# Performance work log

Measured on AMD Instinct MI355X. Metric: run time of the kernel, lower is better.

## Reference

```python
import jax, jax.numpy as jnp
import numpy as np

LN_EPS = 1e-5

def _ln(x, g, b):
    mu = x.mean(-1, keepdims=True)
    var = ((x - mu) ** 2).mean(-1, keepdims=True)
    return (x - mu) * jax.lax.rsqrt(var + LN_EPS) * g + b

def _gru(x, h, wih, whh, bih, bhh):
    # torch GRUCell: gates ordered (r, z, n)
    gi = x @ wih.T + bih
    gh = h @ whh.T + bhh
    ir, iz, inn = jnp.split(gi, 3, axis=-1)
    hr, hz, hn = jnp.split(gh, 3, axis=-1)
    r = jax.nn.sigmoid(ir + hr)
    z = jax.nn.sigmoid(iz + hz)
    n = jnp.tanh(inn + r * hn)
    return (1.0 - z) * n + z * h

def setup_inputs() -> dict:
    key = jax.random.key(0)
    ks = jax.random.split(key, 10)
    B, N, D, S, H = 64, 4096, 128, 8, 256
    w = D ** -0.5  # weight scale to keep activations sane
    return {
        'inputs': jax.random.normal(ks[0], (B, N, D), jnp.float32),
        'slot_noise': jax.random.normal(ks[1], (1, S, D), jnp.float32),
        'slots_mu': jax.random.normal(ks[2], (1, S, D), jnp.float32) * w,
        'slots_log_sigma': jnp.zeros((1, S, D), jnp.float32),
        'wq': jax.random.normal(ks[3], (D, D), jnp.float32) * w,
        'bq': jnp.zeros((D,), jnp.float32),
        'wk': jax.random.normal(ks[4], (D, D), jnp.float32) * w,
        'bk': jnp.zeros((D,), jnp.float32),
        'wv': jax.random.normal(ks[5], (D, D), jnp.float32) * w,
        'bv': jnp.zeros((D,), jnp.float32),
        'gru_wih': jax.random.normal(ks[6], (3 * D, D), jnp.float32) * w,
        'gru_whh': jax.random.normal(ks[7], (3 * D, D), jnp.float32) * w,
        'gru_bih': jnp.zeros((3 * D,), jnp.float32),
        'gru_bhh': jnp.zeros((3 * D,), jnp.float32),
        'ns_g': jnp.ones((D,), jnp.float32),
        'ns_b': jnp.zeros((D,), jnp.float32),
        'ni_g': jnp.ones((D,), jnp.float32),
        'ni_b': jnp.zeros((D,), jnp.float32),
        'mlp_ln_g': jnp.ones((D,), jnp.float32),
        'mlp_ln_b': jnp.zeros((D,), jnp.float32),
        'mlp_w1': jax.random.normal(ks[8], (H, D), jnp.float32) * w,
        'mlp_b1': jnp.zeros((H,), jnp.float32),
        'mlp_w2': jax.random.normal(ks[9], (D, H), jnp.float32) * (H ** -0.5),
        'mlp_b2': jnp.zeros((D,), jnp.float32),
    }

N_ITERS = 3

def reference(inputs, slot_noise, slots_mu, slots_log_sigma, wq, bq, wk, bk, wv, bv,
              gru_wih, gru_whh, gru_bih, gru_bhh, ns_g, ns_b, ni_g, ni_b,
              mlp_ln_g, mlp_ln_b, mlp_w1, mlp_b1, mlp_w2, mlp_b2):
    B, N, D = inputs.shape
    S = slots_mu.shape[1]
    slots = slots_mu + jnp.exp(slots_log_sigma) * slot_noise  # [1,S,D]
    slots = jnp.broadcast_to(slots, (B, S, D))
    x = _ln(inputs, ni_g, ni_b)
    k = x @ wk.T + bk  # [B,N,D]
    v = x @ wv.T + bv
    scale = 1.0 / jnp.sqrt(jnp.float32(D))
    for _ in range(N_ITERS):
        q = _ln(slots, ns_g, ns_b) @ wq.T + bq  # [B,S,D]
        logits = jnp.einsum('bnd,bsd->bns', k, q) * scale
        attn = jax.nn.softmax(logits, axis=-1)  # softmax over slots
        attn_norm = jnp.clip(attn.sum(axis=1, keepdims=True), 1e-8, None)
        slot_attn = attn / attn_norm
        updates = jnp.einsum('bns,bnd->bsd', slot_attn, v)
        slots = _gru(updates, slots, gru_wih, gru_whh, gru_bih, gru_bhh)
        h = jax.nn.gelu(_ln(slots, mlp_ln_g, mlp_ln_b) @ mlp_w1.T + mlp_b1, approximate=False)
        slots = slots + (h @ mlp_w2.T + mlp_b2)
    return slots
```

## Files before the change

kernel.cpp:

```cpp
#include <hip/hip_runtime.h>
#include <hip/hip_bf16.h>
#include <math.h>

#define Bn 64
#define Nn 4096
#define Dn 128
#define Sn 8
#define Hn 256
#define LN_EPS 1e-5f
#define KS_S 136
#define QSCALE 0.08838834764831845f

typedef __bf16 bf16x8 __attribute__((ext_vector_type(8)));
typedef float f32x4 __attribute__((ext_vector_type(4)));
typedef unsigned short ushort_t;

__device__ __forceinline__ float dot4(float4 a, float4 b) {
    return a.x*b.x + a.y*b.y + a.z*b.z + a.w*b.w;
}
__device__ __forceinline__ ushort_t f2bf(float f) {
    __bf16 b = (__bf16)f;
    ushort_t u; __builtin_memcpy(&u, &b, 2); return u;
}
__device__ __forceinline__ float bf2f(ushort_t u) {
    unsigned int x = ((unsigned int)u) << 16; float f; __builtin_memcpy(&f, &x, 4); return f;
}
__device__ __forceinline__ bf16x8 zero8() {
    bf16x8 z;
    #pragma unroll
    for (int i = 0; i < 8; ++i) z[i] = (__bf16)0.0f;
    return z;
}

__global__ void k_slots_init(const float* __restrict__ mu, const float* __restrict__ ls,
                             const float* __restrict__ noise, float* __restrict__ slots) {
    int i = blockIdx.x * blockDim.x + threadIdx.x;
    if (i < Sn * Dn) {
        float v = mu[i] + __expf(ls[i]) * noise[i];
        #pragma unroll 4
        for (int b = 0; b < Bn; ++b) slots[b * Sn * Dn + i] = v;
    }
}

__global__ void k_wprep(const float* __restrict__ wk, const float* __restrict__ wv,
                        ushort_t* __restrict__ wallT) {
    int o = blockIdx.x * blockDim.x + threadIdx.x;
    if (o < 32768) {
        int e = o & 7;
        int l = (o >> 3) & 15;
        int q = (o >> 7) & 3;
        int k = (o >> 9) & 3;
        int G = o >> 11;
        int row = G * 16 + l;
        int col = k * 32 + q * 8 + e;
        float f = (row < 128) ? wk[row * 128 + col] : wv[(row - 128) * 128 + col];
        wallT[o] = f2bf(f);
    }
}

__global__ __launch_bounds__(256) void k_lnkv_mfma(
    const float* __restrict__ inp, const float* __restrict__ ni_g, const float* __restrict__ ni_b,
    const ushort_t* __restrict__ wallT, const float* __restrict__ bk, const float* __restrict__ bv,
    ushort_t* __restrict__ kout, ushort_t* __restrict__ vout)
{
    __shared__ ushort_t xs[64 * KS_S];
    __shared__ float stats[128];
    __shared__ float gb[256];
    const int t = threadIdx.x;
    const int rowbase = blockIdx.x * 64;

    gb[t] = (t < 128) ? ni_g[t] : ni_b[t - 128];

    const float* src = inp + (size_t)rowbase * Dn;
    float4 xv[8];
    #pragma unroll
    for (int it = 0; it < 8; ++it) {
        int f = it * 256 + t;
        float4 x4 = ((const float4*)src)[f];
        xv[it] = x4;
        float s  = x4.x + x4.y + x4.z + x4.w;
        float sq = x4.x*x4.x + x4.y*x4.y + x4.z*x4.z + x4.w*x4.w;
        #pragma unroll
        for (int m = 1; m <= 16; m <<= 1) { s += __shfl_xor(s, m); sq += __shfl_xor(sq, m); }
        if ((t & 31) == 0) {
            int r = it * 8 + (t >> 5);
            float mu  = s * (1.0f / 128.0f);
            float var = sq * (1.0f / 128.0f) - mu * mu;
            stats[2 * r]     = mu;
            stats[2 * r + 1] = rsqrtf(var + LN_EPS);
        }
    }
    __syncthreads();
    #pragma unroll
    for (int it = 0; it < 8; ++it) {
        int f = it * 256 + t;
        int r = f >> 5;
        int c = (f & 31) * 4;
        float mu = stats[2 * r], rs = stats[2 * r + 1];
        float4 x4 = xv[it];
        ushort4 o = { f2bf((x4.x - mu) * rs * gb[c + 0] + gb[128 + c + 0]),
                      f2bf((x4.y - mu) * rs * gb[c + 1] + gb[128 + c + 1]),
                      f2bf((x4.z - mu) * rs * gb[c + 2] + gb[128 + c + 2]),
                      f2bf((x4.w - mu) * rs * gb[c + 3] + gb[128 + c + 3]) };
        *(ushort4*)&xs[r * KS_S + c] = o;
    }
    __syncthreads();

    const int lane = t & 63;
    const int w = t >> 6;
    const int colw = w * 64;
    const int l15 = lane & 15, q = lane >> 4;
    const bool is_k = (colw < 128);
    const int b_idx = rowbase >> 12;
    const int nloc0 = rowbase & 4095;

    bf16x8 afr[4][4];
    #pragma unroll
    for (int ct = 0; ct < 4; ++ct) {
        int G = w * 4 + ct;
        #pragma unroll
        for (int k = 0; k < 4; ++k)
            afr[ct][k] = *(const bf16x8*)&wallT[(size_t)((G * 4 + k) * 64 + lane) * 8];
    }
    float4 biask[4];
    float biasv[4];
    #pragma unroll
    for (int ct = 0; ct < 4; ++ct) {
        if (is_k) biask[ct] = *(const float4*)&bk[colw + ct * 16 + q * 4];
        else      biasv[ct] = bv[colw - 128 + ct * 16 + l15];
    }

    #pragma unroll
    for (int rt = 0; rt < 4; ++rt) {
        bf16x8 bfr[4];
        #pragma unroll
        for (int k = 0; k < 4; ++k)
            bfr[k] = *(const bf16x8*)&xs[(rt * 16 + l15) * KS_S + k * 32 + q * 8];
        #pragma unroll
        for (int ct = 0; ct < 4; ++ct) {
            f32x4 acc = {0.f, 0.f, 0.f, 0.f};
            if (is_k) {
                #pragma unroll
                for (int k = 0; k < 4; ++k)
                    acc = __builtin_amdgcn_mfma_f32_16x16x32_bf16(afr[ct][k], bfr[k], acc, 0, 0, 0);
                int d0 = colw + ct * 16 + q * 4;
                int c  = d0 >> 5;
                int qd = (d0 >> 3) & 3;
                int e0 = d0 & 7;
                ushort4 o = { f2bf(acc[0] + biask[ct].x), f2bf(acc[1] + biask[ct].y),
                              f2bf(acc[2] + biask[ct].z), f2bf(acc[3] + biask[ct].w) };
                size_t off = ((size_t)(((rowbase >> 4) + rt) * 4 + c) * 64 + qd * 16 + l15) * 8 + e0;
                *(ushort4*)&kout[off] = o;
            } else {
                #pragma unroll
                for (int k = 0; k < 4; ++k)
                    acc = __builtin_amdgcn_mfma_f32_16x16x32_bf16(bfr[k], afr[ct][k], acc, 0, 0, 0);
                int dgrp = (w - 2) * 4 + ct;
                int n0 = nloc0 + rt * 16 + q * 4;
                int nc = n0 >> 5;
                int qn = (n0 >> 3) & 3;
                int e0 = n0 & 7;
                float bb = biasv[ct];
                ushort4 o = { f2bf(acc[0] + bb), f2bf(acc[1] + bb),
                              f2bf(acc[2] + bb), f2bf(acc[3] + bb) };
                size_t off = (((size_t)(b_idx * 8 + dgrp) * 128 + nc) * 64 + qn * 16 + l15) * 8 + e0;
                *(ushort4*)&vout[off] = o;
            }
        }
    }
}

__global__ __launch_bounds__(256) void k_qproj2(
    const float* __restrict__ slots, const float* __restrict__ ns_g, const float* __restrict__ ns_b,
    const float* __restrict__ wq, const float* __restrict__ bq,
    ushort_t* __restrict__ qb)
{
    __shared__ float lnq[8][128];
    const int t = threadIdx.x;
    const int bs0 = blockIdx.x * 8;
    {
        int r = t >> 5, c = (t & 31) * 4;
        float4 x4 = *(const float4*)&slots[(size_t)(bs0 + r) * Dn + c];
        float s  = x4.x + x4.y + x4.z + x4.w;
        float sq = x4.x*x4.x + x4.y*x4.y + x4.z*x4.z + x4.w*x4.w;
        #pragma unroll
        for (int m = 1; m <= 16; m <<= 1) { s += __shfl_xor(s, m); sq += __shfl_xor(sq, m); }
        float mu = s * (1.0f / 128.0f);
        float rs = rsqrtf(sq * (1.0f / 128.0f) - mu * mu + LN_EPS);
        lnq[r][c+0] = (x4.x - mu) * rs * ns_g[c+0] + ns_b[c+0];
        lnq[r][c+1] = (x4.y - mu) * rs * ns_g[c+1] + ns_b[c+1];
        lnq[r][c+2] = (x4.z - mu) * rs * ns_g[c+2] + ns_b[c+2];
        lnq[r][c+3] = (x4.w - mu) * rs * ns_g[c+3] + ns_b[c+3];
    }
    __syncthreads();
    {
        int c = t & 127, rb = (t >> 7) * 4;
        const float* W = wq + (size_t)c * Dn;
        float acc[4] = {0.f, 0.f, 0.f, 0.f};
        for (int d = 0; d < 128; d += 4) {
            float4 w4 = *(const float4*)(W + d);
            #pragma unroll
            for (int rr = 0; rr < 4; ++rr) acc[rr] += dot4(w4, *(const float4*)&lnq[rb + rr][d]);
        }
        float bb = bq[c];
        #pragma unroll
        for (int rr = 0; rr < 4; ++rr)
            qb[(size_t)(bs0 + rb + rr) * Dn + c] = f2bf((acc[rr] + bb) * QSCALE);
    }
}

__global__ __launch_bounds__(256) void k_attn_mfma(
    const ushort_t* __restrict__ kbuf, const ushort_t* __restrict__ vtbuf,
    const ushort_t* __restrict__ qb,
    float* __restrict__ upart, float* __restrict__ npart)
{
    __shared__ ushort_t ps[16 * KS_S];
    __shared__ float nsh[8];
    const int t = threadIdx.x;
    const int b = blockIdx.y;
    const int chunk = blockIdx.x;
    const int lane = t & 63;
    const int w = t >> 6;
    const int l15 = lane & 15;
    const int q = lane >> 4;

    for (int i = t; i < 8 * KS_S; i += 256) ps[8 * KS_S + i] = 0;
    if (t < 8) nsh[t] = 0.f;

    bf16x8 aq[4];
    #pragma unroll
    for (int c = 0; c < 4; ++c) {
        bf16x8 z = zero8();
        if (l15 < 8)
            z = *(const bf16x8*)&qb[((size_t)b * Sn + l15) * Dn + c * 32 + q * 8];
        aq[c] = z;
    }

    f32x4 acc[2];
    acc[0] = (f32x4){0.f, 0.f, 0.f, 0.f};
    acc[1] = (f32x4){0.f, 0.f, 0.f, 0.f};
    float nacc[4] = {0.f, 0.f, 0.f, 0.f};

    for (int nt = 0; nt < 4; ++nt) {
        __syncthreads();
        #pragma unroll
        for (int g = 0; g < 2; ++g) {
            int ng = chunk * 32 + nt * 8 + w * 2 + g;
            f32x4 lg = {0.f, 0.f, 0.f, 0.f};
            #pragma unroll
            for (int c = 0; c < 4; ++c) {
                bf16x8 bk = *(const bf16x8*)&kbuf[(((size_t)b * 256 + ng) * 4 + c) * 512 + lane * 8];
                lg = __builtin_amdgcn_mfma_f32_16x16x32_bf16(aq[c], bk, lg, 0, 0, 0);
            }
            int nloc = w * 32 + g * 16 + l15;
            float mown = fmaxf(fmaxf(lg[0], lg[1]), fmaxf(lg[2], lg[3]));
            float m8 = fmaxf(mown, __shfl_xor(mown, 16));
            float p0 = __expf(lg[0] - m8), p1 = __expf(lg[1] - m8);
            float p2 = __expf(lg[2] - m8), p3 = __expf(lg[3] - m8);
            float sown = p0 + p1 + p2 + p3;
            float inv = 1.0f / (sown + __shfl_xor(sown, 16));
            if (q < 2) {
                ushort_t u0 = f2bf(p0 * inv), u1 = f2bf(p1 * inv);
                ushort_t u2 = f2bf(p2 * inv), u3 = f2bf(p3 * inv);
                int s0 = q * 4;
                ps[(s0 + 0) * KS_S + nloc] = u0;
                ps[(s0 + 1) * KS_S + nloc] = u1;
                ps[(s0 + 2) * KS_S + nloc] = u2;
                ps[(s0 + 3) * KS_S + nloc] = u3;
                nacc[0] += bf2f(u0); nacc[1] += bf2f(u1);
                nacc[2] += bf2f(u2); nacc[3] += bf2f(u3);
            }
        }
        __syncthreads();

        bf16x8 pa[4];
        #pragma unroll
        for (int c = 0; c < 4; ++c)
            pa[c] = *(const bf16x8*)&ps[l15 * KS_S + c * 32 + q * 8];

        #pragma unroll
        for (int g2 = 0; g2 < 2; ++g2) {
            int dgrp = w * 2 + g2;
            #pragma unroll
            for (int c = 0; c < 4; ++c) {
                int nc = chunk * 16 + nt * 4 + c;
                bf16x8 bv = *(const bf16x8*)&vtbuf[(((size_t)b * 8 + dgrp) * 128 + nc) * 512 + lane * 8];
                acc[g2] = __builtin_amdgcn_mfma_f32_16x16x32_bf16(pa[c], bv, acc[g2], 0, 0, 0);
            }
        }
    }

    if (q < 2) {
        #pragma unroll
        for (int r = 0; r < 4; ++r) {
            float v = nacc[r];
            v += __shfl_xor(v, 1); v += __shfl_xor(v, 2);
            v += __shfl_xor(v, 4); v += __shfl_xor(v, 8);
            if (l15 == 0) atomicAdd(&nsh[q * 4 + r], v);
        }
        #pragma unroll
        for (int g2 = 0; g2 < 2; ++g2) {
            int d = w * 32 + g2 * 16 + l15;
            #pragma unroll
            for (int r = 0; r < 4; ++r)
                upart[((size_t)(chunk * 64 + b) * 8 + q * 4 + r) * 128 + d] = acc[g2][r];
        }
    }
    __syncthreads();
    if (t < 8) npart[chunk * 512 + b * 8 + t] = nsh[t];
}

__global__ __launch_bounds__(256) void k_update3(
    const float* __restrict__ slots,
    const float* __restrict__ upart, const float* __restrict__ npart,
    const float* __restrict__ wih, const float* __restrict__ whh,
    const float* __restrict__ bih, const float* __restrict__ bhh,
    const float* __restrict__ mlg, const float* __restrict__ mlb,
    const float* __restrict__ w1, const float* __restrict__ b1,
    const float* __restrict__ w2, const float* __restrict__ b2,
    const float* __restrict__ ns_g, const float* __restrict__ ns_b,
    const float* __restrict__ wq, const float* __restrict__ bq,
    float* __restrict__ outp, ushort_t* __restrict__ qb, int do_q)
{
    __shared__ float us[128];
    __shared__ float hs[128];
    __shared__ float gs[768];
    __shared__ float hnw[128];
    __shared__ float lns[128];
    __shared__ float h1s[256];
    const int t = threadIdx.x;
    const int bs = blockIdx.x;

    if (t < 128) {
        float u = 0.f;
        #pragma unroll
        for (int c = 0; c < 8; ++c) u += upart[((size_t)(c * 512 + bs)) * 128 + t];
        float nsum = 0.f;
        #pragma unroll
        for (int c = 0; c < 8; ++c) nsum += npart[c * 512 + bs];
        us[t] = u / fmaxf(nsum, 1e-8f);
        hs[t] = slots[(size_t)bs * Dn + t];
    }
    __syncthreads();

    #pragma unroll
    for (int jj = 0; jj < 3; ++jj) {
        int j = t + jj * 256;
        const float* W = (j < 384) ? (wih + (size_t)j * Dn) : (whh + (size_t)(j - 384) * Dn);
        const float* X = (j < 384) ? us : hs;
        float a = 0.f;
        #pragma unroll 8
        for (int d = 0; d < 128; d += 4)
            a += dot4(*(const float4*)(W + d), *(const float4*)(X + d));
        gs[j] = a;
    }
    __syncthreads();

    if (t < 64) {
        float hnew[2];
        #pragma unroll
        for (int e = 0; e < 2; ++e) {
            int i = t + e * 64;
            float ir = gs[i]       + bih[i],       hr = gs[384 + i] + bhh[i];
            float iz = gs[128 + i] + bih[128 + i], hz = gs[512 + i] + bhh[128 + i];
            float in_= gs[256 + i] + bih[256 + i], hn = gs[640 + i] + bhh[256 + i];
            float r = 1.0f / (1.0f + __expf(-(ir + hr)));
            float z = 1.0f / (1.0f + __expf(-(iz + hz)));
            float n = tanhf(in_ + r * hn);
            hnew[e] = (1.0f - z) * n + z * hs[i];
        }
        float s  = hnew[0] + hnew[1];
        float sq = hnew[0]*hnew[0] + hnew[1]*hnew[1];
        #pragma unroll
        for (int m = 1; m <= 32; m <<= 1) { s += __shfl_xor(s, m); sq += __shfl_xor(sq, m); }
        float mu = s * (1.0f / 128.0f);
        float rs = rsqrtf(sq * (1.0f / 128.0f) - mu * mu + LN_EPS);
        #pragma unroll
        for (int e = 0; e < 2; ++e) {
            int i = t + e * 64;
            hnw[i] = hnew[e];
            lns[i] = (hnew[e] - mu) * rs * mlg[i] + mlb[i];
        }
    }
    __syncthreads();

    {
        const float* W = w1 + (size_t)t * Dn;
        float a = 0.f;
        #pragma unroll 8
        for (int d = 0; d < 128; d += 4)
            a += dot4(*(const float4*)(W + d), *(const float4*)&lns[d]);
        float x = a + b1[t];
        h1s[t] = 0.5f * x * (1.0f + erff(x * 0.70710678118654752f));
    }
    __syncthreads();

    if (t < 128) {
        const float* W = w2 + (size_t)t * Hn;
        float a = 0.f;
        #pragma unroll 8
        for (int d = 0; d < 256; d += 4)
            a += dot4(*(const float4*)(W + d), *(const float4*)&h1s[d]);
        float o = hnw[t] + a + b2[t];
        outp[(size_t)bs * Dn + t] = o;
        us[t] = o;
    }
    if (do_q) {
        __syncthreads();
        if (t < 64) {
            float v0 = us[t], v1 = us[t + 64];
            float s  = v0 + v1;
            float sq = v0*v0 + v1*v1;
            #pragma unroll
            for (int m = 1; m <= 32; m <<= 1) { s += __shfl_xor(s, m); sq += __shfl_xor(sq, m); }
            float mu = s * (1.0f / 128.0f);
            float rs = rsqrtf(sq * (1.0f / 128.0f) - mu * mu + LN_EPS);
            lns[t]      = (v0 - mu) * rs * ns_g[t]      + ns_b[t];
            lns[t + 64] = (v1 - mu) * rs * ns_g[t + 64] + ns_b[t + 64];
        }
        __syncthreads();
        if (t < 128) {
            const float* W = wq + (size_t)t * Dn;
            float a = 0.f;
            #pragma unroll 8
            for (int d = 0; d < 128; d += 4)
                a += dot4(*(const float4*)(W + d), *(const float4*)&lns[d]);
            qb[(size_t)bs * Dn + t] = f2bf((a + bq[t]) * QSCALE);
        }
    }
}

extern "C" void kernel_launch(void* const* d_in, const int* in_sizes, int n_in,
                              void* d_out, int out_size, void* d_ws, size_t ws_size,
                              hipStream_t stream) {
    (void)in_sizes; (void)n_in; (void)out_size; (void)ws_size;
    const float* inputs   = (const float*)d_in[0];
    const float* noise    = (const float*)d_in[1];
    const float* slots_mu = (const float*)d_in[2];
    const float* slots_ls = (const float*)d_in[3];
    const float* wq  = (const float*)d_in[4];
    const float* bq  = (const float*)d_in[5];
    const float* wk  = (const float*)d_in[6];
    const float* bk  = (const float*)d_in[7];
    const float* wv  = (const float*)d_in[8];
    const float* bv  = (const float*)d_in[9];
    const float* gwih = (const float*)d_in[10];
    const float* gwhh = (const float*)d_in[11];
    const float* gbih = (const float*)d_in[12];
    const float* gbhh = (const float*)d_in[13];
    const float* ns_g = (const float*)d_in[14];
    const float* ns_b = (const float*)d_in[15];
    const float* ni_g = (const float*)d_in[16];
    const float* ni_b = (const float*)d_in[17];
    const float* mlg  = (const float*)d_in[18];
    const float* mlb  = (const float*)d_in[19];
    const float* mw1  = (const float*)d_in[20];
    const float* mb1  = (const float*)d_in[21];
    const float* mw2  = (const float*)d_in[22];
    const float* mb2  = (const float*)d_in[23];

    float* ws      = (float*)d_ws;
    float* slots   = ws;
    float* upart   = ws + 65536;
    float* npart   = ws + 590336;
    ushort_t* qb    = (ushort_t*)(ws + 594432);
    ushort_t* wallT = (ushort_t*)(ws + 627200);
    ushort_t* kbuf  = (ushort_t*)(ws + 655360);
    ushort_t* vtbuf = (ushort_t*)(ws + 655360 + 16777216);

    k_slots_init<<<4, 256, 0, stream>>>(slots_mu, slots_ls, noise, slots);
    k_wprep<<<128, 256, 0, stream>>>(wk, wv, wallT);
    k_lnkv_mfma<<<4096, 256, 0, stream>>>(inputs, ni_g, ni_b, wallT, bk, bv, kbuf, vtbuf);
    k_qproj2<<<64, 256, 0, stream>>>(slots, ns_g, ns_b, wq, bq, qb);
    for (int iter = 0; iter < 3; ++iter) {
        k_attn_mfma<<<dim3(8, 64), 256, 0, stream>>>(kbuf, vtbuf, qb, upart, npart);
        float* outp = (iter == 2) ? (float*)d_out : slots;
        k_update3<<<512, 256, 0, stream>>>(slots, upart, npart, gwih, gwhh, gbih, gbhh,
                                           mlg, mlb, mw1, mb1, mw2, mb2, ns_g, ns_b, wq, bq,
                                           outp, qb, (iter == 2) ? 0 : 1);
    }
}
```

Baseline: 481.3 us.

## Keep LN and attention probabilities in registers, drop LDS staging and syncs

The LN+KV projection kernel now has each wave normalise its own 16 rows directly into MFMA B-fragments in registers, instead of staging through LDS. Each wave then loops over all 16 output column tiles, reloading weight fragments from global memory. The attention kernel moves to 512 threads, computes softmax over slots with lane shuffles, and builds the P fragment by shuffles rather than an LDS round trip. Partial updates are reduced across waves in LDS at the end, which removes per-tile barriers and the atomics but adds a larger shared buffer and more weight traffic per block.

```diff
diff --git a/kernel.cpp b/kernel.cpp
--- a/kernel.cpp
+++ b/kernel.cpp
@@ -8,7 +8,6 @@
 #define Sn 8
 #define Hn 256
 #define LN_EPS 1e-5f
-#define KS_S 136
 #define QSCALE 0.08838834764831845f
 
 typedef __bf16 bf16x8 __attribute__((ext_vector_type(8)));
@@ -63,109 +62,82 @@
     const ushort_t* __restrict__ wallT, const float* __restrict__ bk, const float* __restrict__ bv,
     ushort_t* __restrict__ kout, ushort_t* __restrict__ vout)
 {
-    __shared__ ushort_t xs[64 * KS_S];
-    __shared__ float stats[128];
-    __shared__ float gb[256];
     const int t = threadIdx.x;
-    const int rowbase = blockIdx.x * 64;
-
-    gb[t] = (t < 128) ? ni_g[t] : ni_b[t - 128];
-
-    const float* src = inp + (size_t)rowbase * Dn;
-    float4 xv[8];
-    #pragma unroll
-    for (int it = 0; it < 8; ++it) {
-        int f = it * 256 + t;
-        float4 x4 = ((const float4*)src)[f];
-        xv[it] = x4;
-        float s  = x4.x + x4.y + x4.z + x4.w;
-        float sq = x4.x*x4.x + x4.y*x4.y + x4.z*x4.z + x4.w*x4.w;
-        #pragma unroll
-        for (int m = 1; m <= 16; m <<= 1) { s += __shfl_xor(s, m); sq += __shfl_xor(sq, m); }
-        if ((t & 31) == 0) {
-            int r = it * 8 + (t >> 5);
-            float mu  = s * (1.0f / 128.0f);
-            float var = sq * (1.0f / 128.0f) - mu * mu;
-            stats[2 * r]     = mu;
-            stats[2 * r + 1] = rsqrtf(var + LN_EPS);
-        }
-    }
-    __syncthreads();
-    #pragma unroll
-    for (int it = 0; it < 8; ++it) {
-        int f = it * 256 + t;
-        int r = f >> 5;
-        int c = (f & 31) * 4;
-        float mu = stats[2 * r], rs = stats[2 * r + 1];
-        float4 x4 = xv[it];
-        ushort4 o = { f2bf((x4.x - mu) * rs * gb[c + 0] + gb[128 + c + 0]),
-                      f2bf((x4.y - mu) * rs * gb[c + 1] + gb[128 + c + 1]),
-                      f2bf((x4.z - mu) * rs * gb[c + 2] + gb[128 + c + 2]),
-                      f2bf((x4.w - mu) * rs * gb[c + 3] + gb[128 + c + 3]) };
-        *(ushort4*)&xs[r * KS_S + c] = o;
-    }
-    __syncthreads();
-
     const int lane = t & 63;
     const int w = t >> 6;
-    const int colw = w * 64;
     const int l15 = lane & 15, q = lane >> 4;
-    const bool is_k = (colw < 128);
+    const int rowbase = blockIdx.x * 64;
+    const int row = rowbase + w * 16 + l15;
     const int b_idx = rowbase >> 12;
-    const int nloc0 = rowbase & 4095;
-
-    bf16x8 afr[4][4];
-    #pragma unroll
-    for (int ct = 0; ct < 4; ++ct) {
-        int G = w * 4 + ct;
-        #pragma unroll
-        for (int k = 0; k < 4; ++k)
-            afr[ct][k] = *(const bf16x8*)&wallT[(size_t)((G * 4 + k) * 64 + lane) * 8];
-    }
-    float4 biask[4];
-    float biasv[4];
-    #pragma unroll
-    for (int ct = 0; ct < 4; ++ct) {
-        if (is_k) biask[ct] = *(const float4*)&bk[colw + ct * 16 + q * 4];
-        else      biasv[ct] = bv[colw - 128 + ct * 16 + l15];
-    }
-
-    #pragma unroll
-    for (int rt = 0; rt < 4; ++rt) {
-        bf16x8 bfr[4];
-        #pragma unroll
-        for (int k = 0; k < 4; ++k)
-            bfr[k] = *(const bf16x8*)&xs[(rt * 16 + l15) * KS_S + k * 32 + q * 8];
-        #pragma unroll
-        for (int ct = 0; ct < 4; ++ct) {
-            f32x4 acc = {0.f, 0.f, 0.f, 0.f};
-            if (is_k) {
-                #pragma unroll
-                for (int k = 0; k < 4; ++k)
-                    acc = __builtin_amdgcn_mfma_f32_16x16x32_bf16(afr[ct][k], bfr[k], acc, 0, 0, 0);
-                int d0 = colw + ct * 16 + q * 4;
-                int c  = d0 >> 5;
-                int qd = (d0 >> 3) & 3;
-                int e0 = d0 & 7;
-                ushort4 o = { f2bf(acc[0] + biask[ct].x), f2bf(acc[1] + biask[ct].y),
-                              f2bf(acc[2] + biask[ct].z), f2bf(acc[3] + biask[ct].w) };
-                size_t off = ((size_t)(((rowbase >> 4) + rt) * 4 + c) * 64 + qd * 16 + l15) * 8 + e0;
-                *(ushort4*)&kout[off] = o;
-            } else {
-                #pragma unroll
-                for (int k = 0; k < 4; ++k)
-                    acc = __builtin_amdgcn_mfma_f32_16x16x32_bf16(bfr[k], afr[ct][k], acc, 0, 0, 0);
-                int dgrp = (w - 2) * 4 + ct;
-                int n0 = nloc0 + rt * 16 + q * 4;
-                int nc = n0 >> 5;
-                int qn = (n0 >> 3) & 3;
-                int e0 = n0 & 7;
-                float bb = biasv[ct];
-                ushort4 o = { f2bf(acc[0] + bb), f2bf(acc[1] + bb),
-                              f2bf(acc[2] + bb), f2bf(acc[3] + bb) };
-                size_t off = (((size_t)(b_idx * 8 + dgrp) * 128 + nc) * 64 + qn * 16 + l15) * 8 + e0;
-                *(ushort4*)&vout[off] = o;
-            }
+
+    const float* xr = inp + (size_t)row * Dn + q * 8;
+    float4 xv[8];
+    #pragma unroll
+    for (int c = 0; c < 4; ++c) {
+        xv[2*c]   = *(const float4*)(xr + c * 32);
+        xv[2*c+1] = *(const float4*)(xr + c * 32 + 4);
+    }
+    float s = 0.f, sq = 0.f;
+    #pragma unroll
+    for (int i = 0; i < 8; ++i) {
+        float4 x4 = xv[i];
+        s  += x4.x + x4.y + x4.z + x4.w;
+        sq += x4.x*x4.x + x4.y*x4.y + x4.z*x4.z + x4.w*x4.w;
+    }
+    s  += __shfl_xor(s, 16);  s  += __shfl_xor(s, 32);
+    sq += __shfl_xor(sq, 16); sq += __shfl_xor(sq, 32);
+    float mu = s * (1.0f / 128.0f);
+    float rs = rsqrtf(sq * (1.0f / 128.0f) - mu * mu + LN_EPS);
+
+    bf16x8 xf[4];
+    #pragma unroll
+    for (int c = 0; c < 4; ++c) {
+        const float* gp = ni_g + c * 32 + q * 8;
+        const float* bp = ni_b + c * 32 + q * 8;
+        float4 g0 = *(const float4*)gp, g1 = *(const float4*)(gp + 4);
+        float4 b0 = *(const float4*)bp, b1 = *(const float4*)(bp + 4);
+        bf16x8 f;
+        f[0] = (__bf16)((xv[2*c].x   - mu) * rs * g0.x + b0.x);
+        f[1] = (__bf16)((xv[2*c].y   - mu) * rs * g0.y + b0.y);
+        f[2] = (__bf16)((xv[2*c].z   - mu) * rs * g0.z + b0.z);
+        f[3] = (__bf16)((xv[2*c].w   - mu) * rs * g0.w + b0.w);
+        f[4] = (__bf16)((xv[2*c+1].x - mu) * rs * g1.x + b1.x);
+        f[5] = (__bf16)((xv[2*c+1].y - mu) * rs * g1.y + b1.y);
+        f[6] = (__bf16)((xv[2*c+1].z - mu) * rs * g1.z + b1.z);
+        f[7] = (__bf16)((xv[2*c+1].w - mu) * rs * g1.w + b1.w);
+        xf[c] = f;
+    }
+
+    const int nloc0 = (rowbase & 4095) + w * 16 + q * 4;
+    #pragma unroll
+    for (int ct = 0; ct < 16; ++ct) {
+        bf16x8 af[4];
+        #pragma unroll
+        for (int k4 = 0; k4 < 4; ++k4)
+            af[k4] = *(const bf16x8*)&wallT[(size_t)((ct * 4 + k4) * 64 + lane) * 8];
+        f32x4 acc = {0.f, 0.f, 0.f, 0.f};
+        if (ct < 8) {
+            #pragma unroll
+            for (int k4 = 0; k4 < 4; ++k4)
+                acc = __builtin_amdgcn_mfma_f32_16x16x32_bf16(af[k4], xf[k4], acc, 0, 0, 0);
+            int d0 = ct * 16 + q * 4;
+            float4 bia = *(const float4*)&bk[d0];
+            ushort4 o = { f2bf(acc[0] + bia.x), f2bf(acc[1] + bia.y),
+                          f2bf(acc[2] + bia.z), f2bf(acc[3] + bia.w) };
+            size_t off = ((size_t)(((rowbase >> 4) + w) * 4 + (d0 >> 5)) * 64
+                          + ((d0 >> 3) & 3) * 16 + l15) * 8 + (d0 & 7);
+            *(ushort4*)&kout[off] = o;
+        } else {
+            #pragma unroll
+            for (int k4 = 0; k4 < 4; ++k4)
+                acc = __builtin_amdgcn_mfma_f32_16x16x32_bf16(xf[k4], af[k4], acc, 0, 0, 0);
+            int dgrp = ct - 8;
+            float bb = bv[dgrp * 16 + l15];
+            ushort4 o = { f2bf(acc[0] + bb), f2bf(acc[1] + bb),
+                          f2bf(acc[2] + bb), f2bf(acc[3] + bb) };
+            size_t off = (((size_t)(b_idx * 8 + dgrp) * 128 + (nloc0 >> 5)) * 64
+                          + ((nloc0 >> 3) & 3) * 16 + l15) * 8 + (nloc0 & 7);
+            *(ushort4*)&vout[off] = o;
         }
     }
 }
@@ -209,23 +181,21 @@
     }
 }
 
-__global__ __launch_bounds__(256) void k_attn_mfma(
+__global__ __launch_bounds__(512) void k_attn_mfma(
     const ushort_t* __restrict__ kbuf, const ushort_t* __restrict__ vtbuf,
     const ushort_t* __restrict__ qb,
     float* __restrict__ upart, float* __restrict__ npart)
 {
-    __shared__ ushort_t ps[16 * KS_S];
-    __shared__ float nsh[8];
+    __shared__ float ush[8][8][128];
+    __shared__ float nsh[8][8];
     const int t = threadIdx.x;
     const int b = blockIdx.y;
     const int chunk = blockIdx.x;
     const int lane = t & 63;
     const int w = t >> 6;
-    const int l15 = lane & 15;
-    const int q = lane >> 4;
-
-    for (int i = t; i < 8 * KS_S; i += 256) ps[8 * KS_S + i] = 0;
-    if (t < 8) nsh[t] = 0.f;
+    const int l15 = lane & 15, q = lane >> 4;
+    const int srcA = ((lane & 16) << 1) | l15;
+    const bool hi = lane >= 32;
 
     bf16x8 aq[4];
     #pragma unroll
@@ -236,78 +206,89 @@
         aq[c] = z;
     }
 
-    f32x4 acc[2];
-    acc[0] = (f32x4){0.f, 0.f, 0.f, 0.f};
-    acc[1] = (f32x4){0.f, 0.f, 0.f, 0.f};
-    float nacc[4] = {0.f, 0.f, 0.f, 0.f};
-
-    for (int nt = 0; nt < 4; ++nt) {
-        __syncthreads();
-        #pragma unroll
-        for (int g = 0; g < 2; ++g) {
-            int ng = chunk * 32 + nt * 8 + w * 2 + g;
+    f32x4 acc[8];
+    #pragma unroll
+    for (int dg = 0; dg < 8; ++dg) acc[dg] = (f32x4){0.f, 0.f, 0.f, 0.f};
+    float nacc = 0.f;
+
+    #pragma unroll
+    for (int u = 0; u < 2; ++u) {
+        const int n32 = chunk * 512 + w * 64 + u * 32;
+        const int ng = n32 >> 4;
+        float p0[4], p1[4];
+        #pragma unroll
+        for (int T = 0; T < 2; ++T) {
             f32x4 lg = {0.f, 0.f, 0.f, 0.f};
             #pragma unroll
             for (int c = 0; c < 4; ++c) {
-                bf16x8 bk = *(const bf16x8*)&kbuf[(((size_t)b * 256 + ng) * 4 + c) * 512 + lane * 8];
-                lg = __builtin_amdgcn_mfma_f32_16x16x32_bf16(aq[c], bk, lg, 0, 0, 0);
+                bf16x8 kf = *(const bf16x8*)&kbuf[(((size_t)b * 256 + ng + T) * 4 + c) * 512 + lane * 8];
+                lg = __builtin_amdgcn_mfma_f32_16x16x32_bf16(kf, aq[c], lg, 0, 0, 0);
             }
-            int nloc = w * 32 + g * 16 + l15;
-            float mown = fmaxf(fmaxf(lg[0], lg[1]), fmaxf(lg[2], lg[3]));
-            float m8 = fmaxf(mown, __shfl_xor(mown, 16));
-            float p0 = __expf(lg[0] - m8), p1 = __expf(lg[1] - m8);
-            float p2 = __expf(lg[2] - m8), p3 = __expf(lg[3] - m8);
-            float sown = p0 + p1 + p2 + p3;
-            float inv = 1.0f / (sown + __shfl_xor(sown, 16));
-            if (q < 2) {
-                ushort_t u0 = f2bf(p0 * inv), u1 = f2bf(p1 * inv);
-                ushort_t u2 = f2bf(p2 * inv), u3 = f2bf(p3 * inv);
-                int s0 = q * 4;
-                ps[(s0 + 0) * KS_S + nloc] = u0;
-                ps[(s0 + 1) * KS_S + nloc] = u1;
-                ps[(s0 + 2) * KS_S + nloc] = u2;
-                ps[(s0 + 3) * KS_S + nloc] = u3;
-                nacc[0] += bf2f(u0); nacc[1] += bf2f(u1);
-                nacc[2] += bf2f(u2); nacc[3] += bf2f(u3);
+            float* pp = T ? p1 : p0;
+            #pragma unroll
+            for (int r = 0; r < 4; ++r) {
+                float m = lg[r];
+                m = fmaxf(m, __shfl_xor(m, 1));
+                m = fmaxf(m, __shfl_xor(m, 2));
+                m = fmaxf(m, __shfl_xor(m, 4));
+                float p = __expf(lg[r] - m);
+                float ss = p;
+                ss += __shfl_xor(ss, 1); ss += __shfl_xor(ss, 2); ss += __shfl_xor(ss, 4);
+                pp[r] = p * (1.0f / ss);
             }
         }
-        __syncthreads();
-
-        bf16x8 pa[4];
-        #pragma unroll
-        for (int c = 0; c < 4; ++c)
-            pa[c] = *(const bf16x8*)&ps[l15 * KS_S + c * 32 + q * 8];
-
-        #pragma unroll
-        for (int g2 = 0; g2 < 2; ++g2) {
-            int dgrp = w * 2 + g2;
-            #pragma unroll
-            for (int c = 0; c < 4; ++c) {
-                int nc = chunk * 16 + nt * 4 + c;
-                bf16x8 bv = *(const bf16x8*)&vtbuf[(((size_t)b * 8 + dgrp) * 128 + nc) * 512 + lane * 8];
-                acc[g2] = __builtin_amdgcn_mfma_f32_16x16x32_bf16(pa[c], bv, acc[g2], 0, 0, 0);
-            }
-        }
-    }
-
+        float paf[8];
+        #pragma unroll
+        for (int r = 0; r < 4; ++r) {
+            float a0 = __shfl(p0[r], srcA);
+            float a1 = __shfl(p1[r], srcA);
+            float c0 = __shfl(p0[r], srcA + 16);
+            float c1 = __shfl(p1[r], srcA + 16);
+            paf[r]     = hi ? a1 : a0;
+            paf[r + 4] = hi ? c1 : c0;
+        }
+        bf16x8 pa;
+        #pragma unroll
+        for (int e = 0; e < 8; ++e) {
+            __bf16 bb = (__bf16)paf[e];
+            pa[e] = bb;
+            nacc += (float)bb;
+        }
+        const int nc = n32 >> 5;
+        #pragma unroll
+        for (int dg = 0; dg < 8; ++dg) {
+            bf16x8 bv = *(const bf16x8*)&vtbuf[(((size_t)b * 8 + dg) * 128 + nc) * 512 + lane * 8];
+            acc[dg] = __builtin_amdgcn_mfma_f32_16x16x32_bf16(pa, bv, acc[dg], 0, 0, 0);
+        }
+    }
+
+    nacc += __shfl_xor(nacc, 16);
+    nacc += __shfl_xor(nacc, 32);
+    if (lane < 8) nsh[w][lane] = nacc;
     if (q < 2) {
         #pragma unroll
-        for (int r = 0; r < 4; ++r) {
-            float v = nacc[r];
-            v += __shfl_xor(v, 1); v += __shfl_xor(v, 2);
-            v += __shfl_xor(v, 4); v += __shfl_xor(v, 8);
-            if (l15 == 0) atomicAdd(&nsh[q * 4 + r], v);
-        }
-        #pragma unroll
-        for (int g2 = 0; g2 < 2; ++g2) {
-            int d = w * 32 + g2 * 16 + l15;
+        for (int dg = 0; dg < 8; ++dg)
             #pragma unroll
             for (int r = 0; r < 4; ++r)
-                upart[((size_t)(chunk * 64 + b) * 8 + q * 4 + r) * 128 + d] = acc[g2][r];
-        }
-    }
-    __syncthreads();
-    if (t < 8) npart[chunk * 512 + b * 8 + t] = nsh[t];
+                ush[w][q * 4 + r][dg * 16 + l15] = acc[dg][r];
+    }
+    __syncthreads();
+    if (t < 256) {
+        int s = t >> 5, d0 = (t & 31) * 4;
+        float4 sum = {0.f, 0.f, 0.f, 0.f};
+        #pragma unroll
+        for (int w8 = 0; w8 < 8; ++w8) {
+            float4 vv = *(const float4*)&ush[w8][s][d0];
+            sum.x += vv.x; sum.y += vv.y; sum.z += vv.z; sum.w += vv.w;
+        }
+        *(float4*)&upart[((size_t)chunk * 512 + b * 8 + s) * 128 + d0] = sum;
+    }
+    if (t < 8) {
+        float sn = 0.f;
+        #pragma unroll
+        for (int w8 = 0; w8 < 8; ++w8) sn += nsh[w8][t];
+        npart[chunk * 512 + b * 8 + t] = sn;
+    }
 }
 
 __global__ __launch_bounds__(256) void k_update3(
@@ -462,18 +443,18 @@
     float* ws      = (float*)d_ws;
     float* slots   = ws;
     float* upart   = ws + 65536;
-    float* npart   = ws + 590336;
-    ushort_t* qb    = (ushort_t*)(ws + 594432);
-    ushort_t* wallT = (ushort_t*)(ws + 627200);
-    ushort_t* kbuf  = (ushort_t*)(ws + 655360);
-    ushort_t* vtbuf = (ushort_t*)(ws + 655360 + 16777216);
+    float* npart   = ws + 589824;
+    ushort_t* qb    = (ushort_t*)(ws + 593920);
+    ushort_t* wallT = (ushort_t*)(ws + 626688);
+    ushort_t* kbuf  = (ushort_t*)(ws + 643072);
+    ushort_t* vtbuf = kbuf + 33554432;
 
     k_slots_init<<<4, 256, 0, stream>>>(slots_mu, slots_ls, noise, slots);
     k_wprep<<<128, 256, 0, stream>>>(wk, wv, wallT);
     k_lnkv_mfma<<<4096, 256, 0, stream>>>(inputs, ni_g, ni_b, wallT, bk, bv, kbuf, vtbuf);
     k_qproj2<<<64, 256, 0, stream>>>(slots, ns_g, ns_b, wq, bq, qb);
     for (int iter = 0; iter < 3; ++iter) {
-        k_attn_mfma<<<dim3(8, 64), 256, 0, stream>>>(kbuf, vtbuf, qb, upart, npart);
+        k_attn_mfma<<<dim3(8, 64), 512, 0, stream>>>(kbuf, vtbuf, qb, upart, npart);
         float* outp = (iter == 2) ? (float*)d_out : slots;
         k_update3<<<512, 256, 0, stream>>>(slots, upart, npart, gwih, gwhh, gbih, gbhh,
                                            mlg, mlb, mw1, mb1, mw2, mb2, ns_g, ns_b, wq, bq,
```

Result: faster. 471.6 us (-2.0%).
